# Kernel optimization log

Hardware: AMD Instinct MI355X
Metric: run time of the kernel (lower is better)

The kernel has to match this reference:

```python
import jax, jax.numpy as jnp
import numpy as np

K = 16  # knn_k
LN_EPS = 1e-5


def _layernorm(x, g, b):
    mu = jnp.mean(x, axis=-1, keepdims=True)
    var = jnp.var(x, axis=-1, keepdims=True)
    return (x - mu) * jax.lax.rsqrt(var + LN_EPS) * g + b


def _mlp_block(x, W1, b1, g, be, W2, b2):
    # Linear -> LayerNorm -> GELU -> Linear (MLPBlock)
    h = x @ W1 + b1
    h = jax.nn.gelu(_layernorm(h, g, be))
    return h @ W2 + b2


def _knn(v):
    # v: [N,3] -> indices of K nearest neighbors [N,K] (self included, as in knn search)
    sq = jnp.sum(v * v, axis=-1)                       # [N]
    d = sq[:, None] + sq[None, :] - 2.0 * (v @ v.T)    # [N,N] squared dists
    return jax.lax.top_k(-d, K)[1]                     # [N,K]


def setup_inputs() -> dict:
    key = jax.random.key(0)
    ks = jax.random.split(key, 8)
    B, N, C_IN, C_OUT, HID = 2, 8192, 32, 64, 128
    E_IN = C_IN + C_IN + 3  # 67
    s = 0.02
    return {
        "vertices": jax.random.normal(ks[0], (B, N, 3), jnp.float32),
        "features": jax.random.normal(ks[1], (B, N, C_IN), jnp.float32),
        "W1": jax.random.normal(ks[2], (E_IN, HID), jnp.float32) * s,
        "b1": jnp.zeros((HID,), jnp.float32),
        "g1": jnp.ones((HID,), jnp.float32),
        "be1": jnp.zeros((HID,), jnp.float32),
        "W2": jax.random.normal(ks[3], (HID, C_OUT), jnp.float32) * s,
        "b2": jnp.zeros((C_OUT,), jnp.float32),
        "Wo1": jax.random.normal(ks[4], (C_OUT, HID), jnp.float32) * s,
        "bo1": jnp.zeros((HID,), jnp.float32),
        "go": jnp.ones((HID,), jnp.float32),
        "beo": jnp.zeros((HID,), jnp.float32),
        "Wo2": jax.random.normal(ks[5], (HID, C_OUT), jnp.float32) * s,
        "bo2": jnp.zeros((C_OUT,), jnp.float32),
    }


def reference(vertices, features, W1, b1, g1, be1, W2, b2,
              Wo1, bo1, go, beo, Wo2, bo2):
    # out_point_feature_type == 'same': output points == input points
    idx = jax.vmap(_knn)(vertices)                                   # [B,N,K]
    gather = jax.vmap(lambda a, i: jnp.take(a, i, axis=0))
    neigh_feat = gather(features, idx)                               # [B,N,K,C]
    neigh_vert = gather(vertices, idx)                               # [B,N,K,3]
    self_feat = jnp.broadcast_to(features[:, :, None, :], neigh_feat.shape)
    rel_pos = neigh_vert - vertices[:, :, None, :]                   # [B,N,K,3]
    edge = jnp.concatenate([neigh_feat, self_feat, rel_pos], axis=-1)  # [B,N,K,2C+3]
    edge = _mlp_block(edge, W1, b1, g1, be1, W2, b2)                 # [B,N,K,C_out]
    out = jnp.mean(edge, axis=2)                                     # 'mean' reduction over K neighbors
    out = _mlp_block(out, Wo1, bo1, go, beo, Wo2, bo2)               # [B,N,C_out]
    return out
```

## Files before the change

kernel.cpp:

```cpp
#include <hip/hip_runtime.h>
#include <hip/hip_bf16.h>
#include <math.h>

#define BATCH 2
#define NPTS  8192
#define CIN   32
#define HID   128
#define COUT  64
#define EIN   67
#define KNN   16

#define TILE  1024
#define CAP   128
#define KMARGIN 1e-3f

typedef unsigned short u16;
typedef unsigned long long u64;
typedef __attribute__((ext_vector_type(8))) short bf16x8;
typedef __attribute__((ext_vector_type(4))) float f32x4;

#if defined(__has_builtin)
#if __has_builtin(__builtin_amdgcn_rcpf)
#define USE_RCPF 1
#endif
#endif

__device__ __forceinline__ u16 f2b(float f) {
    unsigned u = __float_as_uint(f);
    return (u16)((u + 0x7FFFu + ((u >> 16) & 1u)) >> 16);
}
__device__ __forceinline__ unsigned pk2(float a, float b) {
    return (unsigned)f2b(a) | ((unsigned)f2b(b) << 16);
}
__device__ __forceinline__ float gelu_t(float x) {
    float u = 1.5957691216057308f * (x + 0.044715f * x * x * x);
    float ex = __expf(u);
#ifdef USE_RCPF
    return x * ex * __builtin_amdgcn_rcpf(ex + 1.0f);
#else
    return x * ex / (ex + 1.0f);
#endif
}

__device__ __forceinline__ float rank16_of_64(float v, int lane) {
#pragma unroll
    for (int k = 2; k <= 64; k <<= 1) {
#pragma unroll
        for (int j = k >> 1; j > 0; j >>= 1) {
            float o = __shfl_xor(v, j, 64);
            bool lower = (lane & j) == 0;
            bool asc   = (lane & k) == 0;
            float mn = fminf(v, o), mx = fmaxf(v, o);
            v = (lower == asc) ? mn : mx;
        }
    }
    return __shfl(v, 15, 64);
}

__global__ void prep_kernel(const float* __restrict__ verts, float4* __restrict__ pv) {
    int i = blockIdx.x * blockDim.x + threadIdx.x;
    if (i >= BATCH * NPTS) return;
    float x = verts[3 * i], y = verts[3 * i + 1], z = verts[3 * i + 2];
    float sq = __fadd_rn(__fadd_rn(__fmul_rn(x, x), __fmul_rn(y, y)), __fmul_rn(z, z));
    pv[i] = make_float4(x, y, z, sq);
}

__global__ __launch_bounds__(256, 8) void knn9_kernel(const float4* __restrict__ pv,
                                                      int* __restrict__ nbr_out_rows) {
    __shared__ float  bufD[4][2][CAP];
    __shared__ int    bufJ[4][2][CAP];

    const int tid = threadIdx.x, lane = tid & 63, wv = tid >> 6;
    const int pt0 = (blockIdx.x * 4 + wv) * 2;
    const int b = pt0 >> 13, i0 = pt0 & (NPTS - 1);
    const float4* P = pv + (size_t)b * NPTS;

    float4 sp[2];
    float ax[2], ay[2], az[2];
#pragma unroll
    for (int p = 0; p < 2; ++p) {
        sp[p] = P[i0 + p];
        ax[p] = -2.0f * sp[p].x; ay[p] = -2.0f * sp[p].y; az[p] = -2.0f * sp[p].z;
    }

    float mn[2] = {INFINITY, INFINITY};
    for (int t = 0; t < 16; ++t) {
        float4 c0 = P[t * 256 + lane];
        float4 c1 = P[t * 256 + 64 + lane];
        float4 c2 = P[t * 256 + 128 + lane];
        float4 c3 = P[t * 256 + 192 + lane];
#pragma unroll
        for (int p = 0; p < 2; ++p) {
            float f0 = __fmaf_rn(ax[p], c0.x, __fmaf_rn(ay[p], c0.y, __fmaf_rn(az[p], c0.z, c0.w)));
            float f1 = __fmaf_rn(ax[p], c1.x, __fmaf_rn(ay[p], c1.y, __fmaf_rn(az[p], c1.z, c1.w)));
            float f2 = __fmaf_rn(ax[p], c2.x, __fmaf_rn(ay[p], c2.y, __fmaf_rn(az[p], c2.z, c2.w)));
            float f3 = __fmaf_rn(ax[p], c3.x, __fmaf_rn(ay[p], c3.y, __fmaf_rn(az[p], c3.z, c3.w)));
            mn[p] = fminf(fminf(fminf(mn[p], f0), fminf(f1, f2)), f3);
        }
    }

    float tau[2];
#pragma unroll
    for (int p = 0; p < 2; ++p)
        tau[p] = rank16_of_64(mn[p], lane) + KMARGIN;

    int base[2] = {0, 0};
    for (int t = 0; t < 32; ++t) {
        float4 c[4];
#pragma unroll
        for (int k = 0; k < 4; ++k) c[k] = P[t * 256 + k * 64 + lane];
        bool pr[4][2];
        bool anyl = false;
#pragma unroll
        for (int k = 0; k < 4; ++k)
#pragma unroll
            for (int p = 0; p < 2; ++p) {
                float f = __fmaf_rn(ax[p], c[k].x,
                          __fmaf_rn(ay[p], c[k].y,
                          __fmaf_rn(az[p], c[k].z, c[k].w)));
                pr[k][p] = (f <= tau[p]);
                anyl |= pr[k][p];
            }
        if (__ballot(anyl) == 0ull) continue;
#pragma unroll
        for (int k = 0; k < 4; ++k) {
            u64 anyk = __ballot(pr[k][0] | pr[k][1]);
            if (anyk == 0ull) continue;
            int j = t * 256 + k * 64 + lane;
#pragma unroll
            for (int p = 0; p < 2; ++p) {
                u64 mk = __ballot(pr[k][p]);
                if (mk != 0ull) {
                    if (pr[k][p]) {
                        int pos = base[p] + (int)__popcll(mk & ((1ull << lane) - 1ull));
                        if (pos < CAP) bufJ[wv][p][pos] = j;
                    }
                    base[p] += (int)__popcll(mk);
                }
            }
        }
    }

#pragma unroll
    for (int p = 0; p < 2; ++p) {
        int ns = base[p]; ns = (ns > CAP) ? CAP : ns;
        float dloc[2]; int jloc[2];
#pragma unroll
        for (int slot = 0; slot < 2; ++slot) {
            int sidx = slot * 64 + lane;
            bool act = sidx < ns;
            int js = act ? bufJ[wv][p][sidx] : 0;
            float4 cc = P[js];
            float dot = __fmul_rn(sp[p].x, cc.x);
            dot = __fmaf_rn(sp[p].y, cc.y, dot);
            dot = __fmaf_rn(sp[p].z, cc.z, dot);
            float d = __fsub_rn(__fadd_rn(sp[p].w, cc.w), __fmul_rn(2.0f, dot));
            if (act) bufD[wv][p][sidx] = d;
            dloc[slot] = d; jloc[slot] = js;
        }
        int r0 = 0, r1 = 0;
        for (int mm = 0; mm < ns; ++mm) {
            float dm = bufD[wv][p][mm]; int jm = bufJ[wv][p][mm];
            r0 += (dm < dloc[0]) || (dm == dloc[0] && jm < jloc[0]);
            r1 += (dm < dloc[1]) || (dm == dloc[1] && jm < jloc[1]);
        }
        if (lane < ns && r0 < KNN)
            nbr_out_rows[(size_t)(pt0 + p) * 64 + r0] = jloc[0];
        if (64 + lane < ns && r1 < KNN)
            nbr_out_rows[(size_t)(pt0 + p) * 64 + r1] = jloc[1];
    }
}

__global__ __launch_bounds__(256) void knn_kernel(const float* __restrict__ verts,
                                                  int* nbr_out_rows) {
    __shared__ float4 tilebuf[TILE];
    __shared__ float  bufD[4][CAP];
    __shared__ int    bufJ[4][CAP];

    const int tid = threadIdx.x, lane = tid & 63, wv = tid >> 6;
    const int pt = blockIdx.x * 4 + wv;
    const int b = pt >> 13, i = pt & (NPTS - 1);
    const float* vb = verts + (size_t)b * NPTS * 3;

    const float xi = vb[3 * i], yi = vb[3 * i + 1], zi = vb[3 * i + 2];
    const float sqi = __fadd_rn(__fadd_rn(__fmul_rn(xi, xi), __fmul_rn(yi, yi)),
                                __fmul_rn(zi, zi));

    float m_d = INFINITY;
    for (int t = 0; t < NPTS / TILE; ++t) {
        __syncthreads();
        for (int s = 0; s < TILE / 256; ++s) {
            int p = t * TILE + s * 256 + tid;
            float px = vb[3 * p], py = vb[3 * p + 1], pz = vb[3 * p + 2];
            float sq = __fadd_rn(__fadd_rn(__fmul_rn(px, px), __fmul_rn(py, py)),
                                 __fmul_rn(pz, pz));
            tilebuf[s * 256 + tid] = make_float4(px, py, pz, sq);
        }
        __syncthreads();
        for (int it = 0; it < TILE / 64; ++it) {
            float4 c = tilebuf[it * 64 + lane];
            float dot = __fmul_rn(xi, c.x);
            dot = __fmaf_rn(yi, c.y, dot);
            dot = __fmaf_rn(zi, c.z, dot);
            float d = __fsub_rn(__fadd_rn(sqi, c.w), __fmul_rn(2.0f, dot));
            m_d = fminf(m_d, d);
        }
    }
    __shared__ float minv[4][64];
    minv[wv][lane] = m_d;
    __syncthreads();
    int rnk = 0;
    for (int mm = 0; mm < 64; ++mm) {
        float vm = minv[wv][mm];
        rnk += (vm < m_d) || (vm == m_d && mm < lane);
    }
    u64 bal = __ballot(rnk == 15);
    float tau = __shfl(m_d, __ffsll(bal) - 1, 64);

    int base = 0;
    for (int t = 0; t < NPTS / TILE; ++t) {
        __syncthreads();
        for (int s = 0; s < TILE / 256; ++s) {
            int p = t * TILE + s * 256 + tid;
            float px = vb[3 * p], py = vb[3 * p + 1], pz = vb[3 * p + 2];
            float sq = __fadd_rn(__fadd_rn(__fmul_rn(px, px), __fmul_rn(py, py)),
                                 __fmul_rn(pz, pz));
            tilebuf[s * 256 + tid] = make_float4(px, py, pz, sq);
        }
        __syncthreads();
        for (int it = 0; it < TILE / 64; ++it) {
            int jl = it * 64 + lane;
            float4 c = tilebuf[jl];
            float dot = __fmul_rn(xi, c.x);
            dot = __fmaf_rn(yi, c.y, dot);
            dot = __fmaf_rn(zi, c.z, dot);
            float d = __fsub_rn(__fadd_rn(sqi, c.w), __fmul_rn(2.0f, dot));
            bool pred = (d <= tau);
            u64 mask = __ballot(pred);
            if (pred) {
                int pos = base + (int)__popcll(mask & ((1ull << lane) - 1ull));
                if (pos < CAP) { bufD[wv][pos] = d; bufJ[wv][pos] = t * TILE + jl; }
            }
            base += (int)__popcll(mask);
        }
    }
    int ns = (base > CAP) ? CAP : base;
    __syncthreads();
#pragma unroll
    for (int slot = 0; slot < 2; ++slot) {
        int sidx = slot * 64 + lane;
        if (sidx < ns) {
            float ds = bufD[wv][sidx];
            int   js = bufJ[wv][sidx];
            int rank = 0;
            for (int mm = 0; mm < ns; ++mm) {
                float dm = bufD[wv][mm];
                int   jm = bufJ[wv][mm];
                rank += (dm < ds) || (dm == ds && jm < js);
            }
            if (rank < KNN) nbr_out_rows[(size_t)pt * 64 + rank] = js;
        }
    }
}

__global__ __launch_bounds__(256, 2) void edge4_kernel(
    const float* __restrict__ verts, const float* __restrict__ feats,
    const float* __restrict__ W1, const float* __restrict__ b1,
    const float* __restrict__ g1, const float* __restrict__ be1,
    const float* __restrict__ W2, const float* __restrict__ b2,
    const float* __restrict__ Wo1, const float* __restrict__ bo1,
    const float* __restrict__ go_, const float* __restrict__ beo,
    const float* __restrict__ Wo2, const float* __restrict__ bo2,
    float* out)
{
    __shared__ u16 EPw[4][4][64][8];
    __shared__ u16 W1F[3][8][64][8];
    __shared__ float b1s[HID], g1s[HID], be1s[HID];
    __shared__ float b2s[COUT];
    __shared__ float meansh[16][68];

    const int tid  = threadIdx.x;
    const int lane = tid & 63, wv = tid >> 6;
    const int quad = lane >> 4, n16 = lane & 15;

    for (int s = tid; s < 3 * 8 * 64; s += 256) {
        int kt = s >> 9, nt = (s >> 6) & 7, ln = s & 63;
        int q = ln >> 4, nn = ln & 15;
        int col = nt * 16 + nn;
        union { bf16x8 v; unsigned u[4]; } pk;
#pragma unroll
        for (int jj = 0; jj < 4; ++jj) {
            int k0 = kt * 32 + q * 8 + jj * 2;
            float a  = (k0     < EIN) ? W1[(size_t)k0 * HID + col]       : 0.0f;
            float bq = (k0 + 1 < EIN) ? W1[(size_t)(k0 + 1) * HID + col] : 0.0f;
            pk.u[jj] = pk2(a, bq);
        }
        *(bf16x8*)&W1F[kt][nt][ln][0] = pk.v;
    }
    if (tid < HID) { b1s[tid] = b1[tid]; g1s[tid] = g1[tid]; be1s[tid] = be1[tid]; }
    if (tid < COUT) b2s[tid] = b2[tid];

    bf16x8 w2r[4][4];
#pragma unroll
    for (int kt2 = 0; kt2 < 4; ++kt2)
#pragma unroll
        for (int nt2 = 0; nt2 < 4; ++nt2) {
            union { bf16x8 v; unsigned u[4]; } pk;
#pragma unroll
            for (int jj = 0; jj < 4; ++jj) {
                int k0 = kt2 * 32 + quad * 8 + jj * 2;
                int o = nt2 * 16 + n16;
                pk.u[jj] = pk2(W2[(size_t)k0 * COUT + o],
                               W2[(size_t)(k0 + 1) * COUT + o]);
            }
            w2r[kt2][nt2] = pk.v;
        }
    __syncthreads();

    const int ptb = blockIdx.x * 16;
    const int bb  = ptb >> 13;
    const float* fb  = feats + (size_t)bb * NPTS * CIN;
    const float* vbk = verts + (size_t)bb * NPTS * 3;
    const int ptw = ptb + wv * 4;
    const int ipw = ptw & (NPTS - 1);

    float b1v[8], g1v[8], bev[8];
#pragma unroll
    for (int nt = 0; nt < 8; ++nt) {
        b1v[nt] = b1s[nt * 16 + n16];
        g1v[nt] = g1s[nt * 16 + n16];
        bev[nt] = be1s[nt * 16 + n16];
    }

    const int k16 = lane & 15;
    const int qq  = lane >> 4;

    int jnv[4];
#pragma unroll
    for (int pp = 0; pp < 4; ++pp)
        jnv[pp] = ((const int*)out)[(size_t)(ptw + pp) * 64 + k16];

#pragma unroll
    for (int pp = 0; pp < 4; ++pp) {
        const int jn  = jnv[pp];
        const int ipn = ipw + pp;

        {
            const float* nsrc = fb + (size_t)jn * CIN + qq * 8;
            float4 nA = *(const float4*)nsrc, nB = *(const float4*)(nsrc + 4);
            const float* ssrc = fb + (size_t)ipn * CIN + qq * 8;
            float4 sA = *(const float4*)ssrc, sB = *(const float4*)(ssrc + 4);

            union { bf16x8 v; unsigned u[4]; } e0, e1, e2;
            e0.u[0] = pk2(nA.x, nA.y); e0.u[1] = pk2(nA.z, nA.w);
            e0.u[2] = pk2(nB.x, nB.y); e0.u[3] = pk2(nB.z, nB.w);
            e1.u[0] = pk2(sA.x, sA.y); e1.u[1] = pk2(sA.z, sA.w);
            e1.u[2] = pk2(sB.x, sB.y); e1.u[3] = pk2(sB.z, sB.w);
            e2.u[0] = e2.u[1] = e2.u[2] = e2.u[3] = 0u;
            if (qq == 0) {
                float rx = vbk[3 * jn]     - vbk[3 * ipn];
                float ry = vbk[3 * jn + 1] - vbk[3 * ipn + 1];
                float rz = vbk[3 * jn + 2] - vbk[3 * ipn + 2];
                e2.u[0] = pk2(rx, ry); e2.u[1] = pk2(rz, 0.0f);
            }
            *(bf16x8*)&EPw[wv][0][lane][0] = e0.v;
            *(bf16x8*)&EPw[wv][1][lane][0] = e1.v;
            *(bf16x8*)&EPw[wv][2][lane][0] = e2.v;
        }

        f32x4 acc[8];
#pragma unroll
        for (int nt = 0; nt < 8; ++nt) acc[nt] = (f32x4){0.f, 0.f, 0.f, 0.f};
#pragma unroll
        for (int kt = 0; kt < 3; ++kt) {
            bf16x8 a = *(bf16x8*)&EPw[wv][kt][lane][0];
#pragma unroll
            for (int nt = 0; nt < 8; ++nt) {
                bf16x8 bfr = *(bf16x8*)&W1F[kt][nt][lane][0];
                acc[nt] = __builtin_amdgcn_mfma_f32_16x16x32_bf16(a, bfr, acc[nt], 0, 0, 0);
            }
        }

        float s1[4] = {0,0,0,0}, s2[4] = {0,0,0,0};
#pragma unroll
        for (int nt = 0; nt < 8; ++nt)
#pragma unroll
            for (int r = 0; r < 4; ++r) {
                float x = acc[nt][r] + b1v[nt];
                s1[r] += x; s2[r] += x * x;
            }
#pragma unroll
        for (int r = 0; r < 4; ++r) {
#pragma unroll
            for (int off = 1; off < 16; off <<= 1) {
                s1[r] += __shfl_xor(s1[r], off, 64);
                s2[r] += __shfl_xor(s2[r], off, 64);
            }
        }
        float mu[4], rs[4];
#pragma unroll
        for (int r = 0; r < 4; ++r) {
            mu[r] = s1[r] * (1.0f / HID);
            float var = s2[r] * (1.0f / HID) - mu[r] * mu[r];
            rs[r] = rsqrtf(var + 1e-5f);
        }

#pragma unroll
        for (int nt = 0; nt < 8; ++nt) {
            int kt2 = nt >> 1;
            int q2  = (nt * 2 + (n16 >> 3)) & 3;
            int jj  = n16 & 7;
#pragma unroll
            for (int r = 0; r < 4; ++r) {
                float x  = acc[nt][r] + b1v[nt];
                float xn = (x - mu[r]) * rs[r] * g1v[nt] + bev[nt];
                EPw[wv][kt2][quad * 4 + r + 16 * q2][jj] = (u16)f2b(gelu_t(xn));
            }
        }

        f32x4 acc2[4];
#pragma unroll
        for (int nt2 = 0; nt2 < 4; ++nt2) acc2[nt2] = (f32x4){0.f, 0.f, 0.f, 0.f};
#pragma unroll
        for (int kt2 = 0; kt2 < 4; ++kt2) {
            bf16x8 a2 = *(bf16x8*)&EPw[wv][kt2][lane][0];
#pragma unroll
            for (int nt2 = 0; nt2 < 4; ++nt2)
                acc2[nt2] = __builtin_amdgcn_mfma_f32_16x16x32_bf16(a2, w2r[kt2][nt2], acc2[nt2], 0, 0, 0);
        }

#pragma unroll
        for (int nt2 = 0; nt2 < 4; ++nt2) {
            float cs = acc2[nt2][0] + acc2[nt2][1] + acc2[nt2][2] + acc2[nt2][3];
            cs += __shfl_xor(cs, 16, 64);
            cs += __shfl_xor(cs, 32, 64);
            if (quad == 0) {
                int o = nt2 * 16 + n16;
                meansh[wv * 4 + pp][o] = cs * (1.0f / KNN) + b2s[o];
            }
        }
    }

    __syncthreads();

    for (int s = tid; s < 2 * 8 * 64; s += 256) {
        int kt = s >> 9, nt = (s >> 6) & 7, ln = s & 63;
        int q = ln >> 4, nn = ln & 15;
        int col = nt * 16 + nn;
        union { bf16x8 v; unsigned u[4]; } pk;
#pragma unroll
        for (int jj = 0; jj < 4; ++jj) {
            int k0 = kt * 32 + q * 8 + jj * 2;
            pk.u[jj] = pk2(Wo1[(size_t)k0 * HID + col],
                           Wo1[(size_t)(k0 + 1) * HID + col]);
        }
        *(bf16x8*)&W1F[kt][nt][ln][0] = pk.v;
    }
    if (tid < HID) { b1s[tid] = bo1[tid]; g1s[tid] = go_[tid]; be1s[tid] = beo[tid]; }
    if (tid < COUT) b2s[tid] = bo2[tid];
#pragma unroll
    for (int kt2 = 0; kt2 < 4; ++kt2)
#pragma unroll
        for (int nt2 = 0; nt2 < 4; ++nt2) {
            union { bf16x8 v; unsigned u[4]; } pk;
#pragma unroll
            for (int jj = 0; jj < 4; ++jj) {
                int k0 = kt2 * 32 + quad * 8 + jj * 2;
                int o = nt2 * 16 + n16;
                pk.u[jj] = pk2(Wo2[(size_t)k0 * COUT + o],
                               Wo2[(size_t)(k0 + 1) * COUT + o]);
            }
            w2r[kt2][nt2] = pk.v;
        }
    __syncthreads();

    if (wv == 0) {
        bf16x8 af[2];
#pragma unroll
        for (int kt = 0; kt < 2; ++kt) {
            const float* mrow = &meansh[n16][kt * 32 + quad * 8];
            float4 A = *(const float4*)mrow, B4 = *(const float4*)(mrow + 4);
            union { bf16x8 v; unsigned u[4]; } pk;
            pk.u[0] = pk2(A.x, A.y); pk.u[1] = pk2(A.z, A.w);
            pk.u[2] = pk2(B4.x, B4.y); pk.u[3] = pk2(B4.z, B4.w);
            af[kt] = pk.v;
        }

        f32x4 acc[8];
#pragma unroll
        for (int nt = 0; nt < 8; ++nt) acc[nt] = (f32x4){0.f, 0.f, 0.f, 0.f};
#pragma unroll
        for (int kt = 0; kt < 2; ++kt)
#pragma unroll
            for (int nt = 0; nt < 8; ++nt) {
                bf16x8 bfr = *(bf16x8*)&W1F[kt][nt][lane][0];
                acc[nt] = __builtin_amdgcn_mfma_f32_16x16x32_bf16(af[kt], bfr, acc[nt], 0, 0, 0);
            }

        float pb1[8], pg1[8], pbe[8];
#pragma unroll
        for (int nt = 0; nt < 8; ++nt) {
            pb1[nt] = b1s[nt * 16 + n16];
            pg1[nt] = g1s[nt * 16 + n16];
            pbe[nt] = be1s[nt * 16 + n16];
        }
        float s1[4] = {0,0,0,0}, s2[4] = {0,0,0,0};
#pragma unroll
        for (int nt = 0; nt < 8; ++nt)
#pragma unroll
            for (int r = 0; r < 4; ++r) {
                float x = acc[nt][r] + pb1[nt];
                s1[r] += x; s2[r] += x * x;
            }
#pragma unroll
        for (int r = 0; r < 4; ++r) {
#pragma unroll
            for (int off = 1; off < 16; off <<= 1) {
                s1[r] += __shfl_xor(s1[r], off, 64);
                s2[r] += __shfl_xor(s2[r], off, 64);
            }
        }
#pragma unroll
        for (int nt = 0; nt < 8; ++nt) {
            int kt2 = nt >> 1;
            int q2  = (nt * 2 + (n16 >> 3)) & 3;
            int jj  = n16 & 7;
#pragma unroll
            for (int r = 0; r < 4; ++r) {
                float mu = s1[r] * (1.0f / HID);
                float var = s2[r] * (1.0f / HID) - mu * mu;
                float rs = rsqrtf(var + 1e-5f);
                float x  = acc[nt][r] + pb1[nt];
                float xn = (x - mu) * rs * pg1[nt] + pbe[nt];
                EPw[0][kt2][quad * 4 + r + 16 * q2][jj] = (u16)f2b(gelu_t(xn));
            }
        }

        f32x4 acc2[4];
#pragma unroll
        for (int nt2 = 0; nt2 < 4; ++nt2) acc2[nt2] = (f32x4){0.f, 0.f, 0.f, 0.f};
#pragma unroll
        for (int kt2 = 0; kt2 < 4; ++kt2) {
            bf16x8 a2 = *(bf16x8*)&EPw[0][kt2][lane][0];
#pragma unroll
            for (int nt2 = 0; nt2 < 4; ++nt2)
                acc2[nt2] = __builtin_amdgcn_mfma_f32_16x16x32_bf16(a2, w2r[kt2][nt2], acc2[nt2], 0, 0, 0);
        }

#pragma unroll
        for (int nt2 = 0; nt2 < 4; ++nt2) {
            int o = nt2 * 16 + n16;
#pragma unroll
            for (int r = 0; r < 4; ++r)
                meansh[quad * 4 + r][o] = acc2[nt2][r] + b2s[o];
        }
    }
    __syncthreads();

    {
        int p = tid >> 4, c = (tid & 15) * 4;
        float4 v = *(const float4*)&meansh[p][c];
        *(float4*)&out[(size_t)(ptb + p) * 64 + c] = v;
    }
}

extern "C" void kernel_launch(void* const* d_in, const int* in_sizes, int n_in,
                              void* d_out, int out_size, void* d_ws, size_t ws_size,
                              hipStream_t stream) {
    const float* verts = (const float*)d_in[0];
    const float* feats = (const float*)d_in[1];
    const float* W1  = (const float*)d_in[2];
    const float* b1  = (const float*)d_in[3];
    const float* g1  = (const float*)d_in[4];
    const float* be1 = (const float*)d_in[5];
    const float* W2  = (const float*)d_in[6];
    const float* b2  = (const float*)d_in[7];
    const float* Wo1 = (const float*)d_in[8];
    const float* bo1 = (const float*)d_in[9];
    const float* go_ = (const float*)d_in[10];
    const float* beo = (const float*)d_in[11];
    const float* Wo2 = (const float*)d_in[12];
    const float* bo2 = (const float*)d_in[13];
    float* out = (float*)d_out;

    (void)in_sizes; (void)n_in; (void)out_size;

    const size_t pv_bytes = (size_t)BATCH * NPTS * sizeof(float4);
    if (ws_size >= pv_bytes) {
        float4* pv = (float4*)d_ws;
        prep_kernel<<<(BATCH * NPTS + 255) / 256, 256, 0, stream>>>(verts, pv);
        knn9_kernel<<<(BATCH * NPTS) / 8, 256, 0, stream>>>(pv, (int*)out);
    } else {
        knn_kernel<<<(BATCH * NPTS) / 4, 256, 0, stream>>>(verts, (int*)out);
    }
    edge4_kernel<<<(BATCH * NPTS) / 16, 256, 0, stream>>>(
        verts, feats, W1, b1, g1, be1, W2, b2,
        Wo1, bo1, go_, beo, Wo2, bo2, out);
}
```

Measured before the change: 208.1 us.

## Compute KNN distances with split-bf16 MFMA and threshold-filter candidates

Adds a KNN kernel that computes squared distances through bf16 MFMA, using hi/lo bf16 splits of coordinates and squared norms packed by a new prep kernel. A first pass over a subset of candidates derives a per-point threshold (16th smallest plus a margin). A second pass collects candidates below that threshold into shared memory, then recomputes exact fp32 distances and ranks them to pick the top 16. This replaces the scalar fp32 distance scan with matrix-core work. It risks incorrect neighbours if the threshold pass misses true neighbours or the candidate count exceeds the cap.

```diff
diff --git a/kernel.cpp b/kernel.cpp
--- a/kernel.cpp
+++ b/kernel.cpp
@@ -13,6 +13,7 @@
 #define TILE  1024
 #define CAP   128
 #define KMARGIN 1e-3f
+#define KM_MFMA 4e-3f
 
 typedef unsigned short u16;
 typedef unsigned long long u64;
@@ -28,6 +29,9 @@
 __device__ __forceinline__ u16 f2b(float f) {
     unsigned u = __float_as_uint(f);
     return (u16)((u + 0x7FFFu + ((u >> 16) & 1u)) >> 16);
+}
+__device__ __forceinline__ float b2f(u16 h) {
+    return __uint_as_float(((unsigned)h) << 16);
 }
 __device__ __forceinline__ unsigned pk2(float a, float b) {
     return (unsigned)f2b(a) | ((unsigned)f2b(b) << 16);
@@ -63,6 +67,157 @@
     float x = verts[3 * i], y = verts[3 * i + 1], z = verts[3 * i + 2];
     float sq = __fadd_rn(__fadd_rn(__fmul_rn(x, x), __fmul_rn(y, y)), __fmul_rn(z, z));
     pv[i] = make_float4(x, y, z, sq);
+}
+
+__global__ void prep2_kernel(const float* __restrict__ verts,
+                             float4* __restrict__ pv, uint4* __restrict__ bfrag) {
+    int i = blockIdx.x * blockDim.x + threadIdx.x;
+    if (i >= BATCH * NPTS) return;
+    float x = verts[3 * i], y = verts[3 * i + 1], z = verts[3 * i + 2];
+    float sq = __fadd_rn(__fadd_rn(__fmul_rn(x, x), __fmul_rn(y, y)), __fmul_rn(z, z));
+    pv[i] = make_float4(x, y, z, sq);
+
+    u16 xh = f2b(x);  u16 xl = f2b(x - b2f(xh));
+    u16 yh = f2b(y);  u16 yl = f2b(y - b2f(yh));
+    u16 zh = f2b(z);  u16 zl = f2b(z - b2f(zh));
+    u16 ch = f2b(sq); u16 cl = f2b(sq - b2f(ch));
+
+    uint4 lo, hi;
+    lo.x = (unsigned)xh | ((unsigned)xl << 16);
+    lo.y = (unsigned)xh | ((unsigned)yh << 16);
+    lo.z = (unsigned)yl | ((unsigned)yh << 16);
+    lo.w = (unsigned)zh | ((unsigned)zl << 16);
+    hi.x = (unsigned)zh | ((unsigned)ch << 16);
+    hi.y = (unsigned)cl;
+    hi.z = 0u; hi.w = 0u;
+    bfrag[(size_t)i * 2]     = lo;
+    bfrag[(size_t)i * 2 + 1] = hi;
+}
+
+__global__ __launch_bounds__(256, 4) void knn11_kernel(const float4* __restrict__ pv,
+                                                       const uint4* __restrict__ bfrag,
+                                                       int* __restrict__ nbr_out_rows) {
+    __shared__ float mnsh[4][16][17];
+    __shared__ float taus[16];
+    __shared__ int   cnt[16];
+    __shared__ int   sJ[16][CAP];
+    __shared__ float bufD[16][CAP];
+
+    const int tid = threadIdx.x, lane = tid & 63, wv = tid >> 6;
+    const int col = lane & 15, qq = lane >> 4;
+    const int ptb = blockIdx.x * 16;
+    const int b = ptb >> 13, i0 = ptb & (NPTS - 1);
+    const float4* __restrict__ P = pv + (size_t)b * NPTS;
+    const uint4* __restrict__ BF = bfrag + (size_t)b * NPTS * 2;
+
+    union U { uint4 u; bf16x8 v; };
+
+    union { bf16x8 v; unsigned w[4]; } A;
+    {
+        float4 s = P[i0 + col];
+        float mx = -2.0f * s.x, my = -2.0f * s.y, mz = -2.0f * s.z;
+        u16 mxh = f2b(mx); u16 mxl = f2b(mx - b2f(mxh));
+        u16 myh = f2b(my); u16 myl = f2b(my - b2f(myh));
+        u16 mzh = f2b(mz); u16 mzl = f2b(mz - b2f(mzh));
+        if (qq == 0) {
+            A.w[0] = (unsigned)mxh | ((unsigned)mxh << 16);
+            A.w[1] = (unsigned)mxl | ((unsigned)myh << 16);
+            A.w[2] = (unsigned)myh | ((unsigned)myl << 16);
+            A.w[3] = (unsigned)mzh | ((unsigned)mzh << 16);
+        } else if (qq == 1) {
+            A.w[0] = (unsigned)mzl | (0x3F80u << 16);
+            A.w[1] = 0x3F80u;
+            A.w[2] = 0u; A.w[3] = 0u;
+        } else {
+            A.w[0] = A.w[1] = A.w[2] = A.w[3] = 0u;
+        }
+    }
+
+    const int cb = wv * 2048;
+
+    float mn0 = INFINITY, mn1 = INFINITY, mn2 = INFINITY, mn3 = INFINITY;
+    for (int t = 0; t < 64; ++t) {
+        U bu; bu.u = BF[(size_t)(cb + t * 16 + col) * 2 + (qq & 1)];
+        f32x4 acc = (f32x4){0.f, 0.f, 0.f, 0.f};
+        acc = __builtin_amdgcn_mfma_f32_16x16x32_bf16(A.v, bu.v, acc, 0, 0, 0);
+        mn0 = fminf(mn0, acc[0]); mn1 = fminf(mn1, acc[1]);
+        mn2 = fminf(mn2, acc[2]); mn3 = fminf(mn3, acc[3]);
+    }
+    mnsh[wv][qq * 4 + 0][col] = mn0;
+    mnsh[wv][qq * 4 + 1][col] = mn1;
+    mnsh[wv][qq * 4 + 2][col] = mn2;
+    mnsh[wv][qq * 4 + 3][col] = mn3;
+    if (tid < 16) cnt[tid] = 0;
+    __syncthreads();
+
+    {
+        float tq[4];
+#pragma unroll
+        for (int q = 0; q < 4; ++q) {
+            const int p = wv * 4 + q;
+            float v = mnsh[lane >> 4][p][lane & 15];
+            tq[q] = rank16_of_64(v, lane) + KM_MFMA;
+        }
+        if (lane == 0) {
+#pragma unroll
+            for (int q = 0; q < 4; ++q) taus[wv * 4 + q] = tq[q];
+        }
+    }
+    __syncthreads();
+
+    float mytau[4];
+#pragma unroll
+    for (int r = 0; r < 4; ++r) mytau[r] = taus[qq * 4 + r];
+
+    for (int t = 0; t < 128; ++t) {
+        const int cbase = cb + t * 16;
+        U bu; bu.u = BF[(size_t)(cbase + col) * 2 + (qq & 1)];
+        f32x4 acc = (f32x4){0.f, 0.f, 0.f, 0.f};
+        acc = __builtin_amdgcn_mfma_f32_16x16x32_bf16(A.v, bu.v, acc, 0, 0, 0);
+        if ((acc[0] <= mytau[0]) | (acc[1] <= mytau[1]) |
+            (acc[2] <= mytau[2]) | (acc[3] <= mytau[3])) {
+#pragma unroll
+            for (int r = 0; r < 4; ++r) {
+                if (acc[r] <= mytau[r]) {
+                    int p = qq * 4 + r;
+                    int pos = atomicAdd(&cnt[p], 1);
+                    if (pos < CAP) sJ[p][pos] = cbase + col;
+                }
+            }
+        }
+    }
+    __syncthreads();
+
+#pragma unroll
+    for (int q = 0; q < 4; ++q) {
+        const int p = wv * 4 + q;
+        int ns = cnt[p]; ns = (ns > CAP) ? CAP : ns;
+        const float4 sp = P[i0 + p];
+        float dl[2]; int jl[2];
+#pragma unroll
+        for (int slot = 0; slot < 2; ++slot) {
+            int sidx = slot * 64 + lane;
+            bool act = sidx < ns;
+            int js = act ? sJ[p][sidx] : 0;
+            float4 cc = P[js];
+            float dot = __fmul_rn(sp.x, cc.x);
+            dot = __fmaf_rn(sp.y, cc.y, dot);
+            dot = __fmaf_rn(sp.z, cc.z, dot);
+            float d = __fsub_rn(__fadd_rn(sp.w, cc.w), __fmul_rn(2.0f, dot));
+            if (act) bufD[p][sidx] = d;
+            dl[slot] = d; jl[slot] = js;
+        }
+        int r0 = 0, r1 = 0;
+        for (int mm = 0; mm < ns; ++mm) {
+            float dm = bufD[p][mm]; int jm = sJ[p][mm];
+            r0 += (dm < dl[0]) || (dm == dl[0] && jm < jl[0]);
+            r1 += (dm < dl[1]) || (dm == dl[1] && jm < jl[1]);
+        }
+        if (lane < ns && r0 < KNN)
+            nbr_out_rows[(size_t)(ptb + p) * 64 + r0] = jl[0];
+        if (64 + lane < ns && r1 < KNN)
+            nbr_out_rows[(size_t)(ptb + p) * 64 + r1] = jl[1];
+    }
 }
 
 __global__ __launch_bounds__(256, 8) void knn9_kernel(const float4* __restrict__ pv,
@@ -586,7 +741,13 @@
     (void)in_sizes; (void)n_in; (void)out_size;
 
     const size_t pv_bytes = (size_t)BATCH * NPTS * sizeof(float4);
-    if (ws_size >= pv_bytes) {
+    const size_t bf_bytes = (size_t)BATCH * NPTS * 32;
+    if (ws_size >= pv_bytes + bf_bytes) {
+        float4* pv = (float4*)d_ws;
+        uint4*  bf = (uint4*)((char*)d_ws + pv_bytes);
+        prep2_kernel<<<(BATCH * NPTS + 255) / 256, 256, 0, stream>>>(verts, pv, bf);
+        knn11_kernel<<<(BATCH * NPTS) / 16, 256, 0, stream>>>(pv, bf, (int*)out);
+    } else if (ws_size >= pv_bytes) {
         float4* pv = (float4*)d_ws;
         prep_kernel<<<(BATCH * NPTS + 255) / 256, 256, 0, stream>>>(verts, pv);
         knn9_kernel<<<(BATCH * NPTS) / 8, 256, 0, stream>>>(pv, (int*)out);
```

Result: no change. 211.6 us (+1.7%).
